# Optimization experiments

Hardware: AMD Instinct MI355X
Metric: run time of the kernel (lower is better)

Reference implementation:

```python
import jax, jax.numpy as jnp
import numpy as np

B, S, D_MODEL, H, D_KV = 2, 2048, 1024, 16, 64
NUM_BUCKETS, MAX_DIST = 32, 128


def _relative_position_bucket(rel_pos, num_buckets=NUM_BUCKETS, max_distance=MAX_DIST):
    # bidirectional (encoder) bucketing, matching T5Attention._relative_position_bucket
    nb = num_buckets // 2
    buckets = (rel_pos > 0).astype(jnp.int32) * nb
    rel = jnp.abs(rel_pos)
    max_exact = nb // 2
    is_small = rel < max_exact
    rel_f = jnp.maximum(rel.astype(jnp.float32), 1.0)  # guard log(0); masked by is_small anyway
    large = max_exact + (
        jnp.log(rel_f / max_exact) / np.log(max_distance / max_exact) * (nb - max_exact)
    ).astype(jnp.int32)
    large = jnp.minimum(large, nb - 1)
    return buckets + jnp.where(is_small, rel, large)


def setup_inputs() -> dict:
    key = jax.random.key(0)
    ks = jax.random.split(key, 6)
    sc = 1.0 / np.sqrt(D_MODEL)
    return {
        "hidden_states": jax.random.normal(ks[0], (B, S, D_MODEL), jnp.float32),
        "Wq": jax.random.normal(ks[1], (D_MODEL, H * D_KV), jnp.float32) * sc,
        "Wk": jax.random.normal(ks[2], (D_MODEL, H * D_KV), jnp.float32) * sc,
        "Wv": jax.random.normal(ks[3], (D_MODEL, H * D_KV), jnp.float32) * sc,
        "Wo": jax.random.normal(ks[4], (H * D_KV, D_MODEL), jnp.float32) * sc,
        "rel_bias_table": jax.random.normal(ks[5], (NUM_BUCKETS, H), jnp.float32),
    }


def reference(hidden_states, Wq, Wk, Wv, Wo, rel_bias_table):
    b, s, _ = hidden_states.shape
    # projections (T5 uses no bias, scale=1.0 in attention)
    q = (hidden_states @ Wq).reshape(b, s, H, D_KV).transpose(0, 2, 1, 3)  # bhsd
    k = (hidden_states @ Wk).reshape(b, s, H, D_KV).transpose(0, 2, 1, 3)
    v = (hidden_states @ Wv).reshape(b, s, H, D_KV).transpose(0, 2, 1, 3)

    # relative position bias: [1, H, S, S]
    ctx = jnp.arange(s)[:, None]
    mem = jnp.arange(s)[None, :]
    buckets = _relative_position_bucket(mem - ctx)          # [S, S]
    pos_bias = rel_bias_table[buckets]                       # [S, S, H]
    pos_bias = pos_bias.transpose(2, 0, 1)[None]             # [1, H, S, S]

    scores = jnp.einsum("bhqd,bhkd->bhqk", q, k) + pos_bias  # scale = 1.0
    probs = jax.nn.softmax(scores, axis=-1)
    attn = jnp.einsum("bhqk,bhkd->bhqd", probs, v)
    attn = attn.transpose(0, 2, 1, 3).reshape(b, s, H * D_KV)
    return attn @ Wo
```

## Files before the change

kernel.cpp:

```cpp
#include <hip/hip_runtime.h>
#include <hip/hip_fp16.h>

#define S_LEN 2048
#define NH 16
#define DK 64
#define DM 1024
#define NB 2
#define QKV_SZ (NB * NH * S_LEN * DK)

typedef _Float16 half8 __attribute__((ext_vector_type(8)));
typedef _Float16 half4v __attribute__((ext_vector_type(4)));
typedef __fp16 fp16x2 __attribute__((ext_vector_type(2)));
typedef float f32x4 __attribute__((ext_vector_type(4)));

static __device__ __forceinline__ half4v pack4(const f32x4 v) {
  fp16x2 lo = __builtin_amdgcn_cvt_pkrtz(v[0], v[1]);
  fp16x2 hi = __builtin_amdgcn_cvt_pkrtz(v[2], v[3]);
  half4v r;
  ((fp16x2*)&r)[0] = lo;
  ((fp16x2*)&r)[1] = hi;
  return r;
}

#define GLL(gp, lp)                                                              \
  __builtin_amdgcn_global_load_lds(                                              \
      (const __attribute__((address_space(1))) unsigned int*)(gp),               \
      (__attribute__((address_space(3))) unsigned int*)(lp), 16, 0, 0)


__global__ __launch_bounds__(256) void conv_f32_f16(const float* __restrict__ in,
                                                    _Float16* __restrict__ out, int n4) {
  int i = blockIdx.x * 256 + threadIdx.x;
  if (i >= n4) return;
  float4 v = ((const float4*)in)[i];
  half4v o;
  o[0] = (_Float16)v.x; o[1] = (_Float16)v.y; o[2] = (_Float16)v.z; o[3] = (_Float16)v.w;
  ((half4v*)out)[i] = o;
}

__global__ __launch_bounds__(256) void transpose_conv(const float* __restrict__ W,
                                                      _Float16* __restrict__ Wt, float scale) {
  __shared__ float tile[32][33];
  int tx = threadIdx.x, ty = threadIdx.y;
  int nx = blockIdx.x * 32 + tx;
  int ky = blockIdx.y * 32;
#pragma unroll
  for (int i = 0; i < 32; i += 8) tile[ty + i][tx] = W[(size_t)(ky + ty + i) * DM + nx];
  __syncthreads();
  int kx = ky + tx;
  int ny = blockIdx.x * 32;
#pragma unroll
  for (int i = 0; i < 32; i += 8)
    Wt[(size_t)(ny + ty + i) * DM + kx] = (_Float16)(tile[tx][ty + i] * scale);
}

__global__ __launch_bounds__(256) void bias_tab_kernel(const float* __restrict__ table,
                                                       float* __restrict__ tab) {
  int i = blockIdx.x * 256 + threadIdx.x;
  if (i >= NH * 4095) return;
  int h = i / 4095, r = i - h * 4095;
  int rel = r - 2047;
  int bucket = rel > 0 ? 16 : 0;
  int a = rel < 0 ? -rel : rel;
  if (a < 8) {
    bucket += a;
  } else {
    int lg = 31 - __clz(a * a);
    int large = 8 + (lg - 6);
    bucket += (large < 15 ? large : 15);
  }
  tab[i] = table[bucket * NH + h] * 1.44269504f;
}

template <int MODE>
__global__ __launch_bounds__(256) void gemm_f16(const _Float16* __restrict__ A,
                                                const _Float16* __restrict__ Bt,
                                                void* __restrict__ Cout,
                                                int M, int N, int K) {
  __shared__ _Float16 As[128 * 32];
  __shared__ _Float16 Bs[128 * 32];
  const int t = threadIdx.x;
  const int m0 = blockIdx.y * 128, n0 = blockIdx.x * 128;
  const int w = t >> 6, lane = t & 63, l15 = lane & 15, quad = lane >> 4;
  const int wr = (w >> 1) * 64, wc = (w & 1) * 64;
  const int swz = (quad ^ (l15 & 3)) * 8;

  f32x4 acc[4][4];
#pragma unroll
  for (int i = 0; i < 4; i++)
#pragma unroll
    for (int j = 0; j < 4; j++) acc[i][j] = (f32x4){0.f, 0.f, 0.f, 0.f};

  for (int k0 = 0; k0 < K; k0 += 32) {
    __syncthreads();
#pragma unroll
    for (int i = 0; i < 2; i++) {
      int id = t + 256 * i;
      int row = id >> 2, c = id & 3;
      int cg = c ^ (row & 3);
      GLL(A + (size_t)(m0 + row) * K + k0 + cg * 8, (char*)As + id * 16);
      GLL(Bt + (size_t)(n0 + row) * K + k0 + cg * 8, (char*)Bs + id * 16);
    }
    __syncthreads();
    half8 af[4], bf[4];
#pragma unroll
    for (int i = 0; i < 4; i++) af[i] = *(const half8*)(As + (wr + i * 16 + l15) * 32 + swz);
#pragma unroll
    for (int i = 0; i < 4; i++) bf[i] = *(const half8*)(Bs + (wc + i * 16 + l15) * 32 + swz);
#pragma unroll
    for (int i = 0; i < 4; i++)
#pragma unroll
      for (int j = 0; j < 4; j++)
        acc[i][j] = __builtin_amdgcn_mfma_f32_16x16x32_f16(af[i], bf[j], acc[i][j], 0, 0, 0);
  }

#pragma unroll
  for (int i = 0; i < 4; i++)
#pragma unroll
    for (int j = 0; j < 4; j++) {
      int row0 = m0 + wr + i * 16 + quad * 4;
      int col = n0 + wc + j * 16 + l15;
      if (MODE == 1) {
#pragma unroll
        for (int r = 0; r < 4; r++)
          ((float*)Cout)[(size_t)(row0 + r) * N + col] = acc[i][j][r];
      } else {
        int which = col >> 10, rem = col & 1023, hh = rem >> 6, dd = rem & 63;
        int bb = row0 >> 11, ss = row0 & 2047;
        _Float16* base = (_Float16*)Cout;
        if (which == 2) {
          *(half4v*)(base + (size_t)2 * QKV_SZ +
                     ((size_t)((bb * NH + hh) * DK + dd)) * S_LEN + ss) = pack4(acc[i][j]);
        } else {
#pragma unroll
          for (int r = 0; r < 4; r++)
            base[(size_t)which * QKV_SZ +
                 ((size_t)((bb * NH + hh) * S_LEN) + ss + r) * DK + dd] = (_Float16)acc[i][j][r];
        }
      }
    }
}

__global__ __launch_bounds__(256, 2) void attn_kernel(
    const _Float16* __restrict__ Q, const _Float16* __restrict__ K,
    const _Float16* __restrict__ Vt, const float* __restrict__ btab,
    _Float16* __restrict__ attn_out) {
  __shared__ _Float16 Ks[2][4096];
  __shared__ _Float16 Vs[2][4096];
  __shared__ _Float16 Ps[4][32 * 72];
  __shared__ float slab[640];

  const int t = threadIdx.x;
  const int Q0 = blockIdx.x * 128;
  const int h = blockIdx.y, b = blockIdx.z;
  const int w = t >> 6, lane = t & 63, l15 = lane & 15, quad = lane >> 4;
  const int qw0 = Q0 + w * 32;

  const _Float16* Qb = Q + (size_t)(b * NH + h) * S_LEN * DK;
  const _Float16* Kb = K + (size_t)(b * NH + h) * S_LEN * DK;
  const _Float16* Vb = Vt + (size_t)(b * NH + h) * S_LEN * DK;

  for (int i = t; i < 635; i += 256) slab[i] = btab[h * 4095 + 1730 + i];

  half8 qf[2][2];
#pragma unroll
  for (int qt = 0; qt < 2; qt++)
#pragma unroll
    for (int dh = 0; dh < 2; dh++)
      qf[qt][dh] = *(const half8*)(Qb + (size_t)(qw0 + qt * 16 + l15) * DK + dh * 32 + quad * 8);

  f32x4 o[2][4];
#pragma unroll
  for (int qt = 0; qt < 2; qt++)
#pragma unroll
    for (int dt = 0; dt < 4; dt++) o[qt][dt] = (f32x4){0.f, 0.f, 0.f, 0.f};
  float m_[2] = {-INFINITY, -INFINITY};
  float l_[2] = {0.f, 0.f};

  auto stage = [&](int kc, int bi) {
#pragma unroll
    for (int i = 0; i < 2; i++) {
      int id = t + 256 * i;
      int row = id >> 3, c = id & 7;
      int cg = c ^ (row & 7);
      GLL(Kb + (size_t)(kc + row) * DK + cg * 8, (char*)(&Ks[bi][0]) + id * 16);
      GLL(Vb + (size_t)row * S_LEN + kc + cg * 8, (char*)(&Vs[bi][0]) + id * 16);
    }
  };

  stage(0, 0);
  __syncthreads();

  for (int k0 = 0; k0 < S_LEN; k0 += 64) {
    const int bi = (k0 >> 6) & 1;
    if (k0 + 64 < S_LEN) stage(k0 + 64, bi ^ 1);

    const int dk0 = k0 - qw0;
    const bool farneg = (dk0 <= -191);
    const bool farpos = (dk0 >= 159);
    const bool nearc = !(farneg || farpos);
    const float cb = farneg ? slab[189] : slab[445];

    f32x4 st[2][4];
    if (nearc) {
#pragma unroll
      for (int qt = 0; qt < 2; qt++)
#pragma unroll
        for (int kt = 0; kt < 4; kt++) {
          int i0 = dk0 + kt * 16 + quad * 4 - qt * 16 - l15 + 317;
          f32x4 v;
          v[0] = slab[i0]; v[1] = slab[i0 + 1]; v[2] = slab[i0 + 2]; v[3] = slab[i0 + 3];
          st[qt][kt] = v;
        }
    } else {
#pragma unroll
      for (int qt = 0; qt < 2; qt++)
#pragma unroll
        for (int kt = 0; kt < 4; kt++) st[qt][kt] = (f32x4){0.f, 0.f, 0.f, 0.f};
    }

    half8 kf[4][2];
#pragma unroll
    for (int kt = 0; kt < 4; kt++)
#pragma unroll
      for (int dh = 0; dh < 2; dh++)
        kf[kt][dh] = *(const half8*)(&Ks[bi][(kt * 16 + l15) * 64 +
                                             (((dh << 2) + quad) ^ (l15 & 7)) * 8]);
#pragma unroll
    for (int qt = 0; qt < 2; qt++)
#pragma unroll
      for (int kt = 0; kt < 4; kt++)
#pragma unroll
        for (int dh = 0; dh < 2; dh++)
          st[qt][kt] = __builtin_amdgcn_mfma_f32_16x16x32_f16(kf[kt][dh], qf[qt][dh],
                                                              st[qt][kt], 0, 0, 0);

#pragma unroll
    for (int qt = 0; qt < 2; qt++) {
      float cm = fmaxf(fmaxf(st[qt][0][0], st[qt][0][1]), fmaxf(st[qt][0][2], st[qt][0][3]));
#pragma unroll
      for (int kt = 1; kt < 4; kt++)
        cm = fmaxf(cm, fmaxf(fmaxf(st[qt][kt][0], st[qt][kt][1]),
                             fmaxf(st[qt][kt][2], st[qt][kt][3])));
      cm = fmaxf(cm, __shfl_xor(cm, 16));
      cm = fmaxf(cm, __shfl_xor(cm, 32));
      float mc = nearc ? cm : cm + cb;
      float mnew = fmaxf(m_[qt], mc);
      float alpha = __builtin_amdgcn_exp2f(m_[qt] - mnew);
      m_[qt] = mnew;
      float msub = nearc ? mnew : mnew - cb;
      l_[qt] *= alpha;
#pragma unroll
      for (int dt = 0; dt < 4; dt++) o[qt][dt] *= alpha;
#pragma unroll
      for (int kt = 0; kt < 4; kt++) {
        f32x4 p;
#pragma unroll
        for (int r = 0; r < 4; r++) p[r] = __builtin_amdgcn_exp2f(st[qt][kt][r] - msub);
        l_[qt] += (p[0] + p[1]) + (p[2] + p[3]);
        *(half4v*)(&Ps[w][(qt * 16 + l15) * 72 + kt * 16 + quad * 4]) = pack4(p);
      }
    }
    __asm__ volatile("s_waitcnt lgkmcnt(0)" ::: "memory");

    half8 pf[2][2], vf[4][2];
#pragma unroll
    for (int qt = 0; qt < 2; qt++)
#pragma unroll
      for (int kh = 0; kh < 2; kh++)
        pf[qt][kh] = *(const half8*)(&Ps[w][(qt * 16 + l15) * 72 + kh * 32 + quad * 8]);
#pragma unroll
    for (int dt = 0; dt < 4; dt++)
#pragma unroll
      for (int kh = 0; kh < 2; kh++)
        vf[dt][kh] = *(const half8*)(&Vs[bi][(dt * 16 + l15) * 64 +
                                             (((kh << 2) + quad) ^ (l15 & 7)) * 8]);
#pragma unroll
    for (int qt = 0; qt < 2; qt++)
#pragma unroll
      for (int dt = 0; dt < 4; dt++)
#pragma unroll
        for (int kh = 0; kh < 2; kh++)
          o[qt][dt] = __builtin_amdgcn_mfma_f32_16x16x32_f16(vf[dt][kh], pf[qt][kh],
                                                             o[qt][dt], 0, 0, 0);
    __syncthreads();
  }

#pragma unroll
  for (int qt = 0; qt < 2; qt++) {
    float lf = l_[qt];
    lf += __shfl_xor(lf, 16);
    lf += __shfl_xor(lf, 32);
    float inv = 1.0f / lf;
    int q = qw0 + qt * 16 + l15;
#pragma unroll
    for (int dt = 0; dt < 4; dt++) {
      f32x4 ov = o[qt][dt] * inv;
      *(half4v*)(attn_out + ((size_t)(b * S_LEN + q)) * DM + h * DK + dt * 16 + quad * 4) =
          pack4(ov);
    }
  }
}

extern "C" void kernel_launch(void* const* d_in, const int* in_sizes, int n_in,
                              void* d_out, int out_size, void* d_ws, size_t ws_size,
                              hipStream_t stream) {
  const float* hs  = (const float*)d_in[0];
  const float* Wq  = (const float*)d_in[1];
  const float* Wk  = (const float*)d_in[2];
  const float* Wv  = (const float*)d_in[3];
  const float* Wo  = (const float*)d_in[4];
  const float* tbl = (const float*)d_in[5];
  float* out = (float*)d_out;
  char* ws = (char*)d_ws;

  _Float16* Xh    = (_Float16*)(ws);
  _Float16* Wqkvt = (_Float16*)(ws + (8u << 20));
  _Float16* Wot   = (_Float16*)(ws + (14u << 20));
  _Float16* Qd    = (_Float16*)(ws + (16u << 20));
  _Float16* Kd    = Qd + (size_t)QKV_SZ;
  _Float16* Vd    = Qd + (size_t)2 * QKV_SZ;
  _Float16* Ah    = (_Float16*)(ws + (40u << 20));
  float*    btab  = (float*)(ws + (48u << 20));

  conv_f32_f16<<<4096, 256, 0, stream>>>(hs, Xh, (NB * S_LEN * DM) / 4);
  dim3 tb(32, 8), tg(32, 32);
  transpose_conv<<<tg, tb, 0, stream>>>(Wq, Wqkvt, 1.44269504f);
  transpose_conv<<<tg, tb, 0, stream>>>(Wk, Wqkvt + 1048576, 1.0f);
  transpose_conv<<<tg, tb, 0, stream>>>(Wv, Wqkvt + 2097152, 1.0f);
  transpose_conv<<<tg, tb, 0, stream>>>(Wo, Wot, 1.0f);
  bias_tab_kernel<<<256, 256, 0, stream>>>(tbl, btab);

  gemm_f16<0><<<dim3(24, 32), 256, 0, stream>>>(Xh, Wqkvt, (void*)Qd, NB * S_LEN, 3 * DM, DM);
  attn_kernel<<<dim3(S_LEN / 128, NH, NB), 256, 0, stream>>>(Qd, Kd, Vd, btab, Ah);
  gemm_f16<1><<<dim3(8, 32), 256, 0, stream>>>(Ah, Wot, (void*)out, NB * S_LEN, DM, DM);
}
```

Before: 221.7 us.

## Shrink attention tile to 64 queries, single-buffer K/V, merge weight transposes

The attention kernel now gives each wave 16 query rows instead of 32, halves the block's query tile, drops K/V double buffering, and raises launch bounds to 4 blocks per CU, aiming for higher occupancy and more blocks across the grid. P is stored in a swizzled 64-wide layout, and the online-softmax rescale is skipped when no lane's max increases. The four weight transpose launches are merged into one 3D-grid launch to cut launch overhead. The trade-off is that K/V loads are no longer overlapped within a block and each K/V tile is reused by fewer queries, doubling global K/V traffic.

```diff
diff --git a/kernel.cpp b/kernel.cpp
--- a/kernel.cpp
+++ b/kernel.cpp
@@ -38,9 +38,15 @@
   ((half4v*)out)[i] = o;
 }
 
-__global__ __launch_bounds__(256) void transpose_conv(const float* __restrict__ W,
-                                                      _Float16* __restrict__ Wt, float scale) {
+__global__ __launch_bounds__(256) void transpose_conv4(
+    const float* __restrict__ Wq, const float* __restrict__ Wk,
+    const float* __restrict__ Wv, const float* __restrict__ Wo,
+    _Float16* __restrict__ Wqkvt, _Float16* __restrict__ Wot) {
   __shared__ float tile[32][33];
+  int z = blockIdx.z;
+  const float* W = (z == 0) ? Wq : (z == 1) ? Wk : (z == 2) ? Wv : Wo;
+  _Float16* Wt = (z < 3) ? (Wqkvt + (size_t)z * 1048576) : Wot;
+  float scale = (z == 0) ? 1.44269504f : 1.0f;
   int tx = threadIdx.x, ty = threadIdx.y;
   int nx = blockIdx.x * 32 + tx;
   int ky = blockIdx.y * 32;
@@ -141,164 +147,139 @@
     }
 }
 
-__global__ __launch_bounds__(256, 2) void attn_kernel(
+__global__ __launch_bounds__(256, 4) void attn_kernel(
     const _Float16* __restrict__ Q, const _Float16* __restrict__ K,
     const _Float16* __restrict__ Vt, const float* __restrict__ btab,
     _Float16* __restrict__ attn_out) {
-  __shared__ _Float16 Ks[2][4096];
-  __shared__ _Float16 Vs[2][4096];
-  __shared__ _Float16 Ps[4][32 * 72];
-  __shared__ float slab[640];
+  __shared__ _Float16 Ks[4096];
+  __shared__ _Float16 Vs[4096];
+  __shared__ _Float16 Ps[4][1024];
+  __shared__ float slab[512];
 
   const int t = threadIdx.x;
-  const int Q0 = blockIdx.x * 128;
+  const int Q0 = blockIdx.x * 64;
   const int h = blockIdx.y, b = blockIdx.z;
   const int w = t >> 6, lane = t & 63, l15 = lane & 15, quad = lane >> 4;
-  const int qw0 = Q0 + w * 32;
+  const int qw0 = Q0 + w * 16;
+  const int sw7 = l15 & 7;
 
   const _Float16* Qb = Q + (size_t)(b * NH + h) * S_LEN * DK;
   const _Float16* Kb = K + (size_t)(b * NH + h) * S_LEN * DK;
   const _Float16* Vb = Vt + (size_t)(b * NH + h) * S_LEN * DK;
 
-  for (int i = t; i < 635; i += 256) slab[i] = btab[h * 4095 + 1730 + i];
-
-  half8 qf[2][2];
-#pragma unroll
-  for (int qt = 0; qt < 2; qt++)
-#pragma unroll
-    for (int dh = 0; dh < 2; dh++)
-      qf[qt][dh] = *(const half8*)(Qb + (size_t)(qw0 + qt * 16 + l15) * DK + dh * 32 + quad * 8);
-
-  f32x4 o[2][4];
-#pragma unroll
-  for (int qt = 0; qt < 2; qt++)
-#pragma unroll
-    for (int dt = 0; dt < 4; dt++) o[qt][dt] = (f32x4){0.f, 0.f, 0.f, 0.f};
-  float m_[2] = {-INFINITY, -INFINITY};
-  float l_[2] = {0.f, 0.f};
-
-  auto stage = [&](int kc, int bi) {
+  for (int i = t; i < 512; i += 256) slab[i] = btab[h * 4095 + 1791 + i];
+
+  half8 qf[2];
+#pragma unroll
+  for (int dh = 0; dh < 2; dh++)
+    qf[dh] = *(const half8*)(Qb + (size_t)(qw0 + l15) * DK + dh * 32 + quad * 8);
+
+  f32x4 o[4];
+#pragma unroll
+  for (int dt = 0; dt < 4; dt++) o[dt] = (f32x4){0.f, 0.f, 0.f, 0.f};
+  float m_ = -INFINITY, l_ = 0.f;
+
+  for (int k0 = 0; k0 < S_LEN; k0 += 64) {
 #pragma unroll
     for (int i = 0; i < 2; i++) {
       int id = t + 256 * i;
       int row = id >> 3, c = id & 7;
       int cg = c ^ (row & 7);
-      GLL(Kb + (size_t)(kc + row) * DK + cg * 8, (char*)(&Ks[bi][0]) + id * 16);
-      GLL(Vb + (size_t)row * S_LEN + kc + cg * 8, (char*)(&Vs[bi][0]) + id * 16);
-    }
-  };
-
-  stage(0, 0);
-  __syncthreads();
-
-  for (int k0 = 0; k0 < S_LEN; k0 += 64) {
-    const int bi = (k0 >> 6) & 1;
-    if (k0 + 64 < S_LEN) stage(k0 + 64, bi ^ 1);
+      GLL(Kb + (size_t)(k0 + row) * DK + cg * 8, (char*)Ks + id * 16);
+      GLL(Vb + (size_t)row * S_LEN + k0 + cg * 8, (char*)Vs + id * 16);
+    }
+    __syncthreads();
 
     const int dk0 = k0 - qw0;
     const bool farneg = (dk0 <= -191);
-    const bool farpos = (dk0 >= 159);
+    const bool farpos = (dk0 >= 143);
     const bool nearc = !(farneg || farpos);
-    const float cb = farneg ? slab[189] : slab[445];
-
-    f32x4 st[2][4];
+    const float cb = farneg ? slab[128] : slab[384];
+
+    f32x4 st[4];
     if (nearc) {
 #pragma unroll
-      for (int qt = 0; qt < 2; qt++)
-#pragma unroll
-        for (int kt = 0; kt < 4; kt++) {
-          int i0 = dk0 + kt * 16 + quad * 4 - qt * 16 - l15 + 317;
-          f32x4 v;
-          v[0] = slab[i0]; v[1] = slab[i0 + 1]; v[2] = slab[i0 + 2]; v[3] = slab[i0 + 3];
-          st[qt][kt] = v;
-        }
+      for (int kt = 0; kt < 4; kt++) {
+        int i0 = dk0 + kt * 16 + quad * 4 - l15 + 256;
+        f32x4 v;
+        v[0] = slab[i0]; v[1] = slab[i0 + 1]; v[2] = slab[i0 + 2]; v[3] = slab[i0 + 3];
+        st[kt] = v;
+      }
     } else {
 #pragma unroll
-      for (int qt = 0; qt < 2; qt++)
-#pragma unroll
-        for (int kt = 0; kt < 4; kt++) st[qt][kt] = (f32x4){0.f, 0.f, 0.f, 0.f};
-    }
-
-    half8 kf[4][2];
+      for (int kt = 0; kt < 4; kt++) st[kt] = (f32x4){0.f, 0.f, 0.f, 0.f};
+    }
+
+    half8 kf[4][2], vf[4][2];
 #pragma unroll
     for (int kt = 0; kt < 4; kt++)
 #pragma unroll
       for (int dh = 0; dh < 2; dh++)
-        kf[kt][dh] = *(const half8*)(&Ks[bi][(kt * 16 + l15) * 64 +
-                                             (((dh << 2) + quad) ^ (l15 & 7)) * 8]);
-#pragma unroll
-    for (int qt = 0; qt < 2; qt++)
-#pragma unroll
-      for (int kt = 0; kt < 4; kt++)
-#pragma unroll
-        for (int dh = 0; dh < 2; dh++)
-          st[qt][kt] = __builtin_amdgcn_mfma_f32_16x16x32_f16(kf[kt][dh], qf[qt][dh],
-                                                              st[qt][kt], 0, 0, 0);
-
-#pragma unroll
-    for (int qt = 0; qt < 2; qt++) {
-      float cm = fmaxf(fmaxf(st[qt][0][0], st[qt][0][1]), fmaxf(st[qt][0][2], st[qt][0][3]));
-#pragma unroll
-      for (int kt = 1; kt < 4; kt++)
-        cm = fmaxf(cm, fmaxf(fmaxf(st[qt][kt][0], st[qt][kt][1]),
-                             fmaxf(st[qt][kt][2], st[qt][kt][3])));
-      cm = fmaxf(cm, __shfl_xor(cm, 16));
-      cm = fmaxf(cm, __shfl_xor(cm, 32));
-      float mc = nearc ? cm : cm + cb;
-      float mnew = fmaxf(m_[qt], mc);
-      float alpha = __builtin_amdgcn_exp2f(m_[qt] - mnew);
-      m_[qt] = mnew;
-      float msub = nearc ? mnew : mnew - cb;
-      l_[qt] *= alpha;
-#pragma unroll
-      for (int dt = 0; dt < 4; dt++) o[qt][dt] *= alpha;
-#pragma unroll
-      for (int kt = 0; kt < 4; kt++) {
-        f32x4 p;
-#pragma unroll
-        for (int r = 0; r < 4; r++) p[r] = __builtin_amdgcn_exp2f(st[qt][kt][r] - msub);
-        l_[qt] += (p[0] + p[1]) + (p[2] + p[3]);
-        *(half4v*)(&Ps[w][(qt * 16 + l15) * 72 + kt * 16 + quad * 4]) = pack4(p);
-      }
-    }
+        kf[kt][dh] = *(const half8*)(&Ks[(kt * 16 + l15) * 64 + (((dh << 2) + quad) ^ sw7) * 8]);
+#pragma unroll
+    for (int dt = 0; dt < 4; dt++)
+#pragma unroll
+      for (int kh = 0; kh < 2; kh++)
+        vf[dt][kh] = *(const half8*)(&Vs[(dt * 16 + l15) * 64 + (((kh << 2) + quad) ^ sw7) * 8]);
+
+#pragma unroll
+    for (int kt = 0; kt < 4; kt++)
+#pragma unroll
+      for (int dh = 0; dh < 2; dh++)
+        st[kt] = __builtin_amdgcn_mfma_f32_16x16x32_f16(kf[kt][dh], qf[dh], st[kt], 0, 0, 0);
+
+    float cm = fmaxf(fmaxf(st[0][0], st[0][1]), fmaxf(st[0][2], st[0][3]));
+#pragma unroll
+    for (int kt = 1; kt < 4; kt++)
+      cm = fmaxf(cm, fmaxf(fmaxf(st[kt][0], st[kt][1]), fmaxf(st[kt][2], st[kt][3])));
+    cm = fmaxf(cm, __shfl_xor(cm, 16));
+    cm = fmaxf(cm, __shfl_xor(cm, 32));
+    float mc = nearc ? cm : cm + cb;
+    if (__any(mc > m_)) {
+      float mnew = fmaxf(m_, mc);
+      float alpha = __builtin_amdgcn_exp2f(m_ - mnew);
+      m_ = mnew;
+      l_ *= alpha;
+#pragma unroll
+      for (int dt = 0; dt < 4; dt++) o[dt] *= alpha;
+    }
+    float msub = nearc ? m_ : m_ - cb;
+
+    f32x4 lacc = (f32x4){0.f, 0.f, 0.f, 0.f};
+#pragma unroll
+    for (int kt = 0; kt < 4; kt++) {
+      f32x4 p;
+#pragma unroll
+      for (int r = 0; r < 4; r++) p[r] = __builtin_amdgcn_exp2f(st[kt][r] - msub);
+      lacc += p;
+      int g = 2 * kt + (quad >> 1);
+      *(half4v*)(&Ps[w][l15 * 64 + (g ^ sw7) * 8 + (quad & 1) * 4]) = pack4(p);
+    }
+    l_ += (lacc[0] + lacc[1]) + (lacc[2] + lacc[3]);
     __asm__ volatile("s_waitcnt lgkmcnt(0)" ::: "memory");
 
-    half8 pf[2][2], vf[4][2];
-#pragma unroll
-    for (int qt = 0; qt < 2; qt++)
+    half8 pf[2];
+#pragma unroll
+    for (int kh = 0; kh < 2; kh++)
+      pf[kh] = *(const half8*)(&Ps[w][l15 * 64 + (((kh << 2) + quad) ^ sw7) * 8]);
+#pragma unroll
+    for (int dt = 0; dt < 4; dt++)
 #pragma unroll
       for (int kh = 0; kh < 2; kh++)
-        pf[qt][kh] = *(const half8*)(&Ps[w][(qt * 16 + l15) * 72 + kh * 32 + quad * 8]);
-#pragma unroll
-    for (int dt = 0; dt < 4; dt++)
-#pragma unroll
-      for (int kh = 0; kh < 2; kh++)
-        vf[dt][kh] = *(const half8*)(&Vs[bi][(dt * 16 + l15) * 64 +
-                                             (((kh << 2) + quad) ^ (l15 & 7)) * 8]);
-#pragma unroll
-    for (int qt = 0; qt < 2; qt++)
-#pragma unroll
-      for (int dt = 0; dt < 4; dt++)
-#pragma unroll
-        for (int kh = 0; kh < 2; kh++)
-          o[qt][dt] = __builtin_amdgcn_mfma_f32_16x16x32_f16(vf[dt][kh], pf[qt][kh],
-                                                             o[qt][dt], 0, 0, 0);
+        o[dt] = __builtin_amdgcn_mfma_f32_16x16x32_f16(vf[dt][kh], pf[kh], o[dt], 0, 0, 0);
     __syncthreads();
   }
 
-#pragma unroll
-  for (int qt = 0; qt < 2; qt++) {
-    float lf = l_[qt];
-    lf += __shfl_xor(lf, 16);
-    lf += __shfl_xor(lf, 32);
-    float inv = 1.0f / lf;
-    int q = qw0 + qt * 16 + l15;
-#pragma unroll
-    for (int dt = 0; dt < 4; dt++) {
-      f32x4 ov = o[qt][dt] * inv;
-      *(half4v*)(attn_out + ((size_t)(b * S_LEN + q)) * DM + h * DK + dt * 16 + quad * 4) =
-          pack4(ov);
-    }
+  float lf = l_;
+  lf += __shfl_xor(lf, 16);
+  lf += __shfl_xor(lf, 32);
+  float inv = 1.0f / lf;
+  int q = qw0 + l15;
+#pragma unroll
+  for (int dt = 0; dt < 4; dt++) {
+    f32x4 ov = o[dt] * inv;
+    *(half4v*)(attn_out + ((size_t)(b * S_LEN + q)) * DM + h * DK + dt * 16 + quad * 4) =
+        pack4(ov);
   }
 }
 
@@ -324,14 +305,10 @@
   float*    btab  = (float*)(ws + (48u << 20));
 
   conv_f32_f16<<<4096, 256, 0, stream>>>(hs, Xh, (NB * S_LEN * DM) / 4);
-  dim3 tb(32, 8), tg(32, 32);
-  transpose_conv<<<tg, tb, 0, stream>>>(Wq, Wqkvt, 1.44269504f);
-  transpose_conv<<<tg, tb, 0, stream>>>(Wk, Wqkvt + 1048576, 1.0f);
-  transpose_conv<<<tg, tb, 0, stream>>>(Wv, Wqkvt + 2097152, 1.0f);
-  transpose_conv<<<tg, tb, 0, stream>>>(Wo, Wot, 1.0f);
+  transpose_conv4<<<dim3(32, 32, 4), dim3(32, 8), 0, stream>>>(Wq, Wk, Wv, Wo, Wqkvt, Wot);
   bias_tab_kernel<<<256, 256, 0, stream>>>(tbl, btab);
 
   gemm_f16<0><<<dim3(24, 32), 256, 0, stream>>>(Xh, Wqkvt, (void*)Qd, NB * S_LEN, 3 * DM, DM);
-  attn_kernel<<<dim3(S_LEN / 128, NH, NB), 256, 0, stream>>>(Qd, Kd, Vd, btab, Ah);
+  attn_kernel<<<dim3(S_LEN / 64, NH, NB), 256, 0, stream>>>(Qd, Kd, Vd, btab, Ah);
   gemm_f16<1><<<dim3(8, 32), 256, 0, stream>>>(Ah, Wot, (void*)out, NB * S_LEN, DM, DM);
 }
```

New measurement: 216.8 us. 2.2% less time.
